# Performance work log

Hardware: AMD Instinct MI355X
Metric: run time of the kernel (lower is better)

## Reference

```python
import jax, jax.numpy as jnp
import numpy as np

L, B, D_MODEL, N_STATE = 512, 32, 256, 16
DT_RANK = 16          # ceil(d_model / 16)
D_INNER = D_MODEL     # EXPAND = 1 (required for code self-consistency)


def setup_inputs() -> dict:
    key = jax.random.key(0)
    ks = jax.random.split(key, 6)
    return {
        "position_features": jax.random.normal(ks[0], (L, B, D_MODEL), jnp.float32),
        "flow_features": jax.random.normal(ks[1], (L, B, D_MODEL), jnp.float32),
        "h_state": jnp.zeros((B, D_INNER, N_STATE), jnp.float32),
        "x_proj_w": jax.random.normal(ks[2], (DT_RANK + 2 * N_STATE, D_INNER), jnp.float32) / np.sqrt(D_INNER).astype(np.float32),
        "dt_proj_w": jax.random.normal(ks[3], (D_INNER, DT_RANK), jnp.float32) / np.sqrt(DT_RANK).astype(np.float32),
        "dt_proj_b": jax.random.normal(ks[4], (D_INNER,), jnp.float32) * 0.01,
        "A_log": jnp.log(jnp.broadcast_to(jnp.arange(1, N_STATE + 1, dtype=jnp.float32), (D_INNER, N_STATE))),
        "D_param": jnp.ones((D_INNER,), jnp.float32),
        "out_proj_w": jax.random.normal(ks[5], (D_MODEL, D_INNER), jnp.float32) / np.sqrt(D_INNER).astype(np.float32),
    }


def _forward(position_features, flow_features, h_state,
             x_proj_w, dt_proj_w, dt_proj_b, A_log, D_param, out_proj_w):
    # permute (L, B, d) -> (B, L, d), matching forward()'s permute(1,0,2)
    u = jnp.transpose(position_features, (1, 0, 2))      # (b, l, d_in)
    flow = jnp.transpose(flow_features, (1, 0, 2))       # (b, l, d_in)

    # input-dependent delta, B, C from flow features
    x_dbl = flow @ x_proj_w.T                            # (b, l, dt_rank + 2n)
    delta, Bm, Cm = jnp.split(x_dbl, [DT_RANK, DT_RANK + N_STATE], axis=-1)
    delta = jax.nn.softplus(delta @ dt_proj_w.T + dt_proj_b)   # (b, l, d_in)

    A = -jnp.exp(A_log)                                  # (d_in, n)
    deltaA = jnp.exp(jnp.einsum('bld,dn->bldn', delta, A))         # (b,l,d,n)
    deltaB_u = jnp.einsum('bld,bln,bld->bldn', delta, Bm, u)       # (b,l,d,n)

    # sequential selective scan over l via lax.scan
    dA_t = jnp.swapaxes(deltaA, 0, 1)                    # (l, b, d, n)
    dBu_t = jnp.swapaxes(deltaB_u, 0, 1)                 # (l, b, d, n)
    C_t = jnp.swapaxes(Cm, 0, 1)                         # (l, b, n)

    def step(h, xs):
        dA, dBu, c = xs
        h = dA * h + dBu                                 # (b, d, n)
        y = jnp.einsum('bdn,bn->bd', h, c)               # (b, d)
        return h, y

    h_final, ys = jax.lax.scan(step, h_state, (dA_t, dBu_t, C_t))
    y = jnp.swapaxes(ys, 0, 1)                           # (b, l, d_in)
    y = y + u * D_param                                  # skip connection

    out = y @ out_proj_w.T                               # (b, l, d_model)
    return out.reshape(out.shape[0], -1), h_final        # flatten(1)


def reference(position_features, flow_features, h_state,
              x_proj_w, dt_proj_w, dt_proj_b, A_log, D_param, out_proj_w):
    return _forward(position_features, flow_features, h_state,
                    x_proj_w, dt_proj_w, dt_proj_b, A_log, D_param, out_proj_w)
```

## Files before the change

kernel.cpp:

```cpp
#include <hip/hip_runtime.h>
#include <hip/hip_bf16.h>

#define LL 512
#define BB 32
#define DD 256
#define NS 16
#define RK 16
#define CH 32
#define LC 16

typedef __attribute__((ext_vector_type(8))) short bf16x8;
typedef __attribute__((ext_vector_type(8))) _Float16 f16x8;
typedef __attribute__((ext_vector_type(4))) float f32x4;

#define LD16(dst, src, off) { \
  float4 _v0 = *reinterpret_cast<const float4*>(&(src)[(off)]); \
  float4 _v1 = *reinterpret_cast<const float4*>(&(src)[(off)+4]); \
  float4 _v2 = *reinterpret_cast<const float4*>(&(src)[(off)+8]); \
  float4 _v3 = *reinterpret_cast<const float4*>(&(src)[(off)+12]); \
  dst[0]=_v0.x; dst[1]=_v0.y; dst[2]=_v0.z; dst[3]=_v0.w; \
  dst[4]=_v1.x; dst[5]=_v1.y; dst[6]=_v1.z; dst[7]=_v1.w; \
  dst[8]=_v2.x; dst[9]=_v2.y; dst[10]=_v2.z; dst[11]=_v2.w; \
  dst[12]=_v3.x; dst[13]=_v3.y; dst[14]=_v3.z; dst[15]=_v3.w; }

#define CP16(dst, src) { _Pragma("unroll") for (int _i = 0; _i < 16; ++_i) dst[_i] = src[_i]; }

static __device__ __forceinline__ unsigned short f2bf(float x) {
    __hip_bfloat16 h = __float2bfloat16(x);
    return *reinterpret_cast<unsigned short*>(&h);
}

static __device__ __forceinline__ f16x8 ld_cvt_f16(const float* p) {
    float4 lo = *reinterpret_cast<const float4*>(p);
    float4 hi = *reinterpret_cast<const float4*>(p + 4);
    f16x8 r;
    r[0] = (_Float16)lo.x; r[1] = (_Float16)lo.y; r[2] = (_Float16)lo.z; r[3] = (_Float16)lo.w;
    r[4] = (_Float16)hi.x; r[5] = (_Float16)hi.y; r[6] = (_Float16)hi.z; r[7] = (_Float16)hi.w;
    return r;
}

__global__ __launch_bounds__(256) void k0_wbf(
    const float* __restrict__ W, unsigned short* __restrict__ Wbf)
{
    int i = (blockIdx.x * 256 + threadIdx.x) * 4;
    float4 v = *reinterpret_cast<const float4*>(&W[i]);
    ushort4 o;
    o.x = f2bf(v.x); o.y = f2bf(v.y); o.z = f2bf(v.z); o.w = f2bf(v.w);
    *reinterpret_cast<ushort4*>(&Wbf[i]) = o;
}

__global__ __launch_bounds__(256) void k0_atab(
    const float* __restrict__ A_log, float* __restrict__ atab, float* __restrict__ atabT)
{
    int i = blockIdx.x * 256 + threadIdx.x;
    int d = i >> 4, n = i & 15;
    float v = -__expf(A_log[i]) * 1.44269504f;
    atab[i] = v;
    atabT[n * DD + d] = v;
}

__global__ __launch_bounds__(256) void k1_fused(
    const float* __restrict__ flow,
    const float* __restrict__ xw,
    const float* __restrict__ dtw,
    const float* __restrict__ dtb,
    float* __restrict__ delta,
    float* __restrict__ Bm,
    float* __restrict__ Cm)
{
    __shared__ float sx16[4][16][17];
    int wave = threadIdx.x >> 6;
    int lane = threadIdx.x & 63;
    int rl = lane & 15, kb = lane >> 4;
    int rowbase = blockIdx.x * 64 + wave * 16;
    int arow = rowbase + rl;
    int b = arow >> 9, l = arow & 511;
    const float* abase = &flow[(l * BB + b) * DD];

    f32x4 acc[3] = {};
    #pragma unroll
    for (int ks = 0; ks < 8; ++ks) {
        int k0 = ks * 32 + kb * 8;
        f16x8 af = ld_cvt_f16(abase + k0);
        #pragma unroll
        for (int j = 0; j < 3; ++j) {
            f16x8 bfr = ld_cvt_f16(&xw[(j * 16 + rl) * DD + k0]);
            acc[j] = __builtin_amdgcn_mfma_f32_16x16x32_f16(af, bfr, acc[j], 0, 0, 0);
        }
    }
    #pragma unroll
    for (int reg = 0; reg < 4; ++reg) {
        int row = rowbase + kb * 4 + reg;
        Bm[(size_t)row * NS + rl] = acc[1][reg];
        Cm[(size_t)row * NS + rl] = acc[2][reg];
        sx16[wave][kb * 4 + reg][rl] = acc[0][reg];
    }
    __syncthreads();

    f16x8 a2;
    if (kb < 2) {
        #pragma unroll
        for (int j = 0; j < 8; ++j)
            a2[j] = (_Float16)sx16[wave][rl][kb * 8 + j];
    } else {
        #pragma unroll
        for (int j = 0; j < 8; ++j) a2[j] = (_Float16)0.f;
    }

    #pragma unroll 4
    for (int m = 0; m < 16; ++m) {
        f16x8 b2;
        if (kb < 2) {
            float4 lo = *reinterpret_cast<const float4*>(&dtw[(m * 16 + rl) * RK + kb * 8]);
            float4 hi = *reinterpret_cast<const float4*>(&dtw[(m * 16 + rl) * RK + kb * 8 + 4]);
            b2[0] = (_Float16)lo.x; b2[1] = (_Float16)lo.y; b2[2] = (_Float16)lo.z; b2[3] = (_Float16)lo.w;
            b2[4] = (_Float16)hi.x; b2[5] = (_Float16)hi.y; b2[6] = (_Float16)hi.z; b2[7] = (_Float16)hi.w;
        } else {
            #pragma unroll
            for (int j = 0; j < 8; ++j) b2[j] = (_Float16)0.f;
        }
        f32x4 acc2 = {};
        acc2 = __builtin_amdgcn_mfma_f32_16x16x32_f16(a2, b2, acc2, 0, 0, 0);
        int d = m * 16 + rl;
        float bias = dtb[d];
        #pragma unroll
        for (int reg = 0; reg < 4; ++reg) {
            float s = acc2[reg] + bias;
            float sp = fmaxf(s, 0.f) + log1pf(__expf(-fabsf(s)));
            delta[(size_t)(rowbase + kb * 4 + reg) * DD + d] = sp;
        }
    }
}

__global__ __launch_bounds__(512, 4) void k2A(
    const float* __restrict__ u_pos,
    const float* __restrict__ atab,
    const float* __restrict__ Dp,
    float* __restrict__ delta,
    const float* __restrict__ Bm,
    const float* __restrict__ Cm,
    float* __restrict__ ypart,
    float* __restrict__ hfin,
    float* __restrict__ sfin)
{
    int tid = threadIdx.x;
    int b  = blockIdx.x >> 4;
    int dt = blockIdx.x & 15;
    int dl = tid & 15, c = tid >> 4;
    int d  = dt * 16 + dl;
    int l0 = c * LC;

    float a[NS];
    LD16(a, atab, d * NS);
    float Dd = Dp[d];

    float* dp = delta + ((size_t)b * LL + l0) * DD + d;
    const float* up = u_pos + ((size_t)l0 * BB + b) * DD + d;
    const float* Bp = Bm + ((size_t)b * LL + l0) * NS;
    const float* Cp = Cm + ((size_t)b * LL + l0) * NS;
    float* yp = ypart + ((size_t)b * LL + l0) * DD + d;

    float h[NS];
    #pragma unroll
    for (int n = 0; n < NS; ++n) h[n] = 0.f;
    float s = 0.f;

    float dlt = dp[0], uv = up[0];
    float Bv[NS], Cv[NS];
    LD16(Bv, Bp, 0);
    LD16(Cv, Cp, 0);

    for (int l = 0; l < LC; ++l) {
        int lp = (l + 1 < LC) ? l + 1 : l;
        float dlt_n = dp[lp * DD];
        float uv_n  = up[lp * BB * DD];
        float Bn[NS], Cn[NS];
        LD16(Bn, Bp, lp * NS);
        LD16(Cn, Cp, lp * NS);

        s += dlt;
        float du = dlt * uv;
        float acc = uv * Dd;
        #pragma unroll
        for (int n = 0; n < NS; ++n) {
            float dA = exp2f(dlt * a[n]);
            h[n] = fmaf(dA, h[n], du * Bv[n]);
            acc = fmaf(h[n], Cv[n], acc);
        }
        yp[l * DD] = acc;
        dp[l * DD] = s;

        dlt = dlt_n; uv = uv_n;
        CP16(Bv, Bn); CP16(Cv, Cn);
    }

    sfin[((size_t)b * CH + c) * DD + d] = s;
    #pragma unroll
    for (int n = 0; n < NS; ++n)
        hfin[(((size_t)b * CH + c) * NS + n) * DD + d] = h[n];
}

__global__ __launch_bounds__(256) void k2B(
    const float* __restrict__ h0,
    const float* __restrict__ atabT,
    const float* __restrict__ sfin,
    float* __restrict__ hfin,
    float* __restrict__ h_out)
{
    int d = threadIdx.x;
    int b = blockIdx.x >> 4;
    int n = blockIdx.x & 15;
    float an = atabT[n * DD + d];
    float s = h0[((size_t)b * DD + d) * NS + n];
    #pragma unroll 4
    for (int c = 0; c < CH; ++c) {
        float sf = sfin[((size_t)b * CH + c) * DD + d];
        size_t oh = (((size_t)b * CH + c) * NS + n) * DD + d;
        float hp = hfin[oh];
        hfin[oh] = s;
        s = fmaf(exp2f(an * sf), s, hp);
    }
    h_out[((size_t)b * DD + d) * NS + n] = s;
}

__global__ __launch_bounds__(256) void k2C(
    const float* __restrict__ atabT,
    const float* __restrict__ Slocal,
    const float* __restrict__ Cm,
    const float* __restrict__ hfin,
    const float* __restrict__ ypart,
    unsigned short* __restrict__ ybf)
{
    int d = threadIdx.x;
    int b = blockIdx.x >> 5;
    int c = blockIdx.x & 31;
    int l0 = c * LC;

    float a[NS], hin[NS];
    #pragma unroll
    for (int n = 0; n < NS; ++n) {
        a[n]   = atabT[n * DD + d];
        hin[n] = hfin[(((size_t)b * CH + c) * NS + n) * DD + d];
    }

    size_t base = ((size_t)b * LL + l0) * DD + d;
    const float* CpB = Cm + ((size_t)b * LL + l0) * NS;

    #pragma unroll 2
    for (int l = 0; l < LC; ++l) {
        float Cv[NS];
        LD16(Cv, CpB, l * NS);
        size_t idx = base + (size_t)l * DD;
        float sS = Slocal[idx];
        float acc = ypart[idx];
        #pragma unroll
        for (int n = 0; n < NS; ++n)
            acc = fmaf(exp2f(a[n] * sS), Cv[n] * hin[n], acc);
        ybf[idx] = f2bf(acc);
    }
}

__global__ __launch_bounds__(256) void k3_mfma(
    const unsigned short* __restrict__ Ybf,
    const unsigned short* __restrict__ Wbf,
    float* __restrict__ Out)
{
    int wave = threadIdx.x >> 6;
    int lane = threadIdx.x & 63;
    int row0 = (blockIdx.x >> 1) * 32 + (wave >> 1) * 16;
    int col0 = (blockIdx.x & 1) * 128 + (wave & 1) * 64;
    int rl = lane & 15, kb = lane >> 4;

    f32x4 acc[4] = {};
    bf16x8 af, bf[4], afn, bfn[4];

    af = *reinterpret_cast<const bf16x8*>(&Ybf[(size_t)(row0 + rl) * DD + kb * 8]);
    #pragma unroll
    for (int j = 0; j < 4; ++j)
        bf[j] = *reinterpret_cast<const bf16x8*>(&Wbf[(size_t)(col0 + j * 16 + rl) * DD + kb * 8]);

    #pragma unroll
    for (int ks = 0; ks < 8; ++ks) {
        int kn = (ks + 1) * 32 + kb * 8;
        if (ks < 7) {
            afn = *reinterpret_cast<const bf16x8*>(&Ybf[(size_t)(row0 + rl) * DD + kn]);
            #pragma unroll
            for (int j = 0; j < 4; ++j)
                bfn[j] = *reinterpret_cast<const bf16x8*>(&Wbf[(size_t)(col0 + j * 16 + rl) * DD + kn]);
        }
        #pragma unroll
        for (int j = 0; j < 4; ++j)
            acc[j] = __builtin_amdgcn_mfma_f32_16x16x32_bf16(af, bf[j], acc[j], 0, 0, 0);
        af = afn;
        #pragma unroll
        for (int j = 0; j < 4; ++j) bf[j] = bfn[j];
    }

    #pragma unroll
    for (int j = 0; j < 4; ++j)
        #pragma unroll
        for (int reg = 0; reg < 4; ++reg)
            Out[(size_t)(row0 + kb * 4 + reg) * DD + col0 + j * 16 + rl] = acc[j][reg];
}

extern "C" void kernel_launch(void* const* d_in, const int* in_sizes, int n_in,
                              void* d_out, int out_size, void* d_ws, size_t ws_size,
                              hipStream_t stream) {
    const float* pos  = (const float*)d_in[0];
    const float* flow = (const float*)d_in[1];
    const float* h0   = (const float*)d_in[2];
    const float* xw   = (const float*)d_in[3];
    const float* dtw  = (const float*)d_in[4];
    const float* dtb  = (const float*)d_in[5];
    const float* alog = (const float*)d_in[6];
    const float* dpar = (const float*)d_in[7];
    const float* ow   = (const float*)d_in[8];

    float* out = (float*)d_out;

    float* ws    = (float*)d_ws;
    float* delta = ws;
    float* Bmw   = ws + 4194304;
    float* Cmw   = ws + 4456448;
    float* ypart = ws + 4718592;
    float* hfin  = ws + 8912896;
    float* sfin  = ws + 13107200;
    float* atab  = ws + 13369344;
    float* atabT = ws + 13373440;
    unsigned short* ybf = (unsigned short*)(ws + 13377536);
    unsigned short* wbf = (unsigned short*)(ws + 15474688);

    float* h_out = out + 32 * 512 * 256;

    k0_wbf  <<<64,   256, 0, stream>>>(ow, wbf);
    k0_atab <<<16,   256, 0, stream>>>(alog, atab, atabT);
    k1_fused<<<256,  256, 0, stream>>>(flow, xw, dtw, dtb, delta, Bmw, Cmw);
    k2A     <<<512,  512, 0, stream>>>(pos, atab, dpar, delta, Bmw, Cmw, ypart, hfin, sfin);
    k2B     <<<512,  256, 0, stream>>>(h0, atabT, sfin, hfin, h_out);
    k2C     <<<1024, 256, 0, stream>>>(atabT, delta, Cmw, hfin, ypart, ybf);
    k3_mfma <<<1024, 256, 0, stream>>>(ybf, wbf, out);
}
```

Before: 214.9 us.

## Fuse chunk correction with output GEMM and split scan state across lanes

New measurement: 214.3 us. About the same (-0.3%).

```diff
diff --git a/kernel.cpp b/kernel.cpp
--- a/kernel.cpp
+++ b/kernel.cpp
@@ -8,8 +8,8 @@
 #define RK 16
 #define CH 32
 #define LC 16
-
-typedef __attribute__((ext_vector_type(8))) short bf16x8;
+#define L2E 1.44269504f
+
 typedef __attribute__((ext_vector_type(8))) _Float16 f16x8;
 typedef __attribute__((ext_vector_type(4))) float f32x4;
 
@@ -23,12 +23,11 @@
   dst[8]=_v2.x; dst[9]=_v2.y; dst[10]=_v2.z; dst[11]=_v2.w; \
   dst[12]=_v3.x; dst[13]=_v3.y; dst[14]=_v3.z; dst[15]=_v3.w; }
 
-#define CP16(dst, src) { _Pragma("unroll") for (int _i = 0; _i < 16; ++_i) dst[_i] = src[_i]; }
-
-static __device__ __forceinline__ unsigned short f2bf(float x) {
-    __hip_bfloat16 h = __float2bfloat16(x);
-    return *reinterpret_cast<unsigned short*>(&h);
-}
+#define LD8(dst, src, off) { \
+  float4 _v0 = *reinterpret_cast<const float4*>(&(src)[(off)]); \
+  float4 _v1 = *reinterpret_cast<const float4*>(&(src)[(off)+4]); \
+  dst[0]=_v0.x; dst[1]=_v0.y; dst[2]=_v0.z; dst[3]=_v0.w; \
+  dst[4]=_v1.x; dst[5]=_v1.y; dst[6]=_v1.z; dst[7]=_v1.w; }
 
 static __device__ __forceinline__ f16x8 ld_cvt_f16(const float* p) {
     float4 lo = *reinterpret_cast<const float4*>(p);
@@ -37,26 +36,6 @@
     r[0] = (_Float16)lo.x; r[1] = (_Float16)lo.y; r[2] = (_Float16)lo.z; r[3] = (_Float16)lo.w;
     r[4] = (_Float16)hi.x; r[5] = (_Float16)hi.y; r[6] = (_Float16)hi.z; r[7] = (_Float16)hi.w;
     return r;
-}
-
-__global__ __launch_bounds__(256) void k0_wbf(
-    const float* __restrict__ W, unsigned short* __restrict__ Wbf)
-{
-    int i = (blockIdx.x * 256 + threadIdx.x) * 4;
-    float4 v = *reinterpret_cast<const float4*>(&W[i]);
-    ushort4 o;
-    o.x = f2bf(v.x); o.y = f2bf(v.y); o.z = f2bf(v.z); o.w = f2bf(v.w);
-    *reinterpret_cast<ushort4*>(&Wbf[i]) = o;
-}
-
-__global__ __launch_bounds__(256) void k0_atab(
-    const float* __restrict__ A_log, float* __restrict__ atab, float* __restrict__ atabT)
-{
-    int i = blockIdx.x * 256 + threadIdx.x;
-    int d = i >> 4, n = i & 15;
-    float v = -__expf(A_log[i]) * 1.44269504f;
-    atab[i] = v;
-    atabT[n * DD + d] = v;
 }
 
 __global__ __launch_bounds__(256) void k1_fused(
@@ -134,7 +113,7 @@
 
 __global__ __launch_bounds__(512, 4) void k2A(
     const float* __restrict__ u_pos,
-    const float* __restrict__ atab,
+    const float* __restrict__ A_log,
     const float* __restrict__ Dp,
     float* __restrict__ delta,
     const float* __restrict__ Bm,
@@ -144,65 +123,65 @@
     float* __restrict__ sfin)
 {
     int tid = threadIdx.x;
-    int b  = blockIdx.x >> 4;
-    int dt = blockIdx.x & 15;
-    int dl = tid & 15, c = tid >> 4;
+    int bid = blockIdx.x;
+    int cg = bid & 1;
+    int dt = (bid >> 1) & 15;
+    int b  = bid >> 5;
+    int dl = tid & 15;
+    int nh = (tid >> 4) & 1;
+    int cl = tid >> 5;
+    int c  = cg * 16 + cl;
     int d  = dt * 16 + dl;
     int l0 = c * LC;
 
-    float a[NS];
-    LD16(a, atab, d * NS);
+    float a[8];
+    LD8(a, A_log, d * NS + nh * 8);
+    #pragma unroll
+    for (int n = 0; n < 8; ++n) a[n] = -__expf(a[n]) * L2E;
     float Dd = Dp[d];
 
     float* dp = delta + ((size_t)b * LL + l0) * DD + d;
     const float* up = u_pos + ((size_t)l0 * BB + b) * DD + d;
-    const float* Bp = Bm + ((size_t)b * LL + l0) * NS;
-    const float* Cp = Cm + ((size_t)b * LL + l0) * NS;
+    const float* Bp = Bm + ((size_t)b * LL + l0) * NS + nh * 8;
+    const float* Cp = Cm + ((size_t)b * LL + l0) * NS + nh * 8;
     float* yp = ypart + ((size_t)b * LL + l0) * DD + d;
 
-    float h[NS];
-    #pragma unroll
-    for (int n = 0; n < NS; ++n) h[n] = 0.f;
+    float h[8];
+    #pragma unroll
+    for (int n = 0; n < 8; ++n) h[n] = 0.f;
     float s = 0.f;
 
-    float dlt = dp[0], uv = up[0];
-    float Bv[NS], Cv[NS];
-    LD16(Bv, Bp, 0);
-    LD16(Cv, Cp, 0);
-
     for (int l = 0; l < LC; ++l) {
-        int lp = (l + 1 < LC) ? l + 1 : l;
-        float dlt_n = dp[lp * DD];
-        float uv_n  = up[lp * BB * DD];
-        float Bn[NS], Cn[NS];
-        LD16(Bn, Bp, lp * NS);
-        LD16(Cn, Cp, lp * NS);
-
+        float dlt = dp[l * DD];
+        float uv  = up[l * BB * DD];
+        float Bv[8], Cv[8];
+        LD8(Bv, Bp, l * NS);
+        LD8(Cv, Cp, l * NS);
         s += dlt;
         float du = dlt * uv;
-        float acc = uv * Dd;
-        #pragma unroll
-        for (int n = 0; n < NS; ++n) {
+        float acc = nh ? 0.f : uv * Dd;
+        #pragma unroll
+        for (int n = 0; n < 8; ++n) {
             float dA = exp2f(dlt * a[n]);
             h[n] = fmaf(dA, h[n], du * Bv[n]);
             acc = fmaf(h[n], Cv[n], acc);
         }
-        yp[l * DD] = acc;
-        dp[l * DD] = s;
-
-        dlt = dlt_n; uv = uv_n;
-        CP16(Bv, Bn); CP16(Cv, Cn);
-    }
-
-    sfin[((size_t)b * CH + c) * DD + d] = s;
-    #pragma unroll
-    for (int n = 0; n < NS; ++n)
-        hfin[(((size_t)b * CH + c) * NS + n) * DD + d] = h[n];
+        acc += __shfl_xor(acc, 16);
+        if (!nh) {
+            yp[l * DD] = acc;
+            dp[l * DD] = s;
+        }
+    }
+
+    if (!nh) sfin[((size_t)b * CH + c) * DD + d] = s;
+    #pragma unroll
+    for (int n = 0; n < 8; ++n)
+        hfin[(((size_t)b * CH + c) * NS + nh * 8 + n) * DD + d] = h[n];
 }
 
 __global__ __launch_bounds__(256) void k2B(
     const float* __restrict__ h0,
-    const float* __restrict__ atabT,
+    const float* __restrict__ A_log,
     const float* __restrict__ sfin,
     float* __restrict__ hfin,
     float* __restrict__ h_out)
@@ -210,7 +189,7 @@
     int d = threadIdx.x;
     int b = blockIdx.x >> 4;
     int n = blockIdx.x & 15;
-    float an = atabT[n * DD + d];
+    float an = -__expf(A_log[d * NS + n]) * L2E;
     float s = h0[((size_t)b * DD + d) * NS + n];
     #pragma unroll 4
     for (int c = 0; c < CH; ++c) {
@@ -223,84 +202,70 @@
     h_out[((size_t)b * DD + d) * NS + n] = s;
 }
 
-__global__ __launch_bounds__(256) void k2C(
-    const float* __restrict__ atabT,
+__global__ __launch_bounds__(512) void k23(
+    const float* __restrict__ A_log,
     const float* __restrict__ Slocal,
     const float* __restrict__ Cm,
     const float* __restrict__ hfin,
     const float* __restrict__ ypart,
-    unsigned short* __restrict__ ybf)
-{
-    int d = threadIdx.x;
-    int b = blockIdx.x >> 5;
-    int c = blockIdx.x & 31;
-    int l0 = c * LC;
-
-    float a[NS], hin[NS];
-    #pragma unroll
-    for (int n = 0; n < NS; ++n) {
-        a[n]   = atabT[n * DD + d];
-        hin[n] = hfin[(((size_t)b * CH + c) * NS + n) * DD + d];
-    }
-
-    size_t base = ((size_t)b * LL + l0) * DD + d;
-    const float* CpB = Cm + ((size_t)b * LL + l0) * NS;
-
-    #pragma unroll 2
-    for (int l = 0; l < LC; ++l) {
-        float Cv[NS];
-        LD16(Cv, CpB, l * NS);
-        size_t idx = base + (size_t)l * DD;
-        float sS = Slocal[idx];
-        float acc = ypart[idx];
-        #pragma unroll
-        for (int n = 0; n < NS; ++n)
-            acc = fmaf(exp2f(a[n] * sS), Cv[n] * hin[n], acc);
-        ybf[idx] = f2bf(acc);
-    }
-}
-
-__global__ __launch_bounds__(256) void k3_mfma(
-    const unsigned short* __restrict__ Ybf,
-    const unsigned short* __restrict__ Wbf,
+    const float* __restrict__ W,
     float* __restrict__ Out)
 {
-    int wave = threadIdx.x >> 6;
-    int lane = threadIdx.x & 63;
-    int row0 = (blockIdx.x >> 1) * 32 + (wave >> 1) * 16;
-    int col0 = (blockIdx.x & 1) * 128 + (wave & 1) * 64;
-    int rl = lane & 15, kb = lane >> 4;
-
-    f32x4 acc[4] = {};
-    bf16x8 af, bf[4], afn, bfn[4];
-
-    af = *reinterpret_cast<const bf16x8*>(&Ybf[(size_t)(row0 + rl) * DD + kb * 8]);
-    #pragma unroll
-    for (int j = 0; j < 4; ++j)
-        bf[j] = *reinterpret_cast<const bf16x8*>(&Wbf[(size_t)(col0 + j * 16 + rl) * DD + kb * 8]);
-
-    #pragma unroll
-    for (int ks = 0; ks < 8; ++ks) {
-        int kn = (ks + 1) * 32 + kb * 8;
-        if (ks < 7) {
-            afn = *reinterpret_cast<const bf16x8*>(&Ybf[(size_t)(row0 + rl) * DD + kn]);
+    __shared__ _Float16 sy[32][264];
+    int tid = threadIdx.x;
+    int b  = blockIdx.x >> 4;
+    int rg = blockIdx.x & 15;
+    int l0 = rg * 32;
+
+    {
+        int d = tid & 255, lgrp = tid >> 8;
+        int c = rg * 2 + lgrp;
+        float a[NS], hin[NS];
+        LD16(a, A_log, d * NS);
+        #pragma unroll
+        for (int n = 0; n < NS; ++n) {
+            a[n] = -__expf(a[n]) * L2E;
+            hin[n] = hfin[(((size_t)b * CH + c) * NS + n) * DD + d];
+        }
+        size_t base = ((size_t)b * LL + l0 + lgrp * 16) * DD + d;
+        const float* Cp = Cm + ((size_t)b * LL + l0 + lgrp * 16) * NS;
+        #pragma unroll 2
+        for (int i = 0; i < 16; ++i) {
+            float Cv[NS];
+            LD16(Cv, Cp, i * NS);
+            size_t idx = base + (size_t)i * DD;
+            float sS = Slocal[idx];
+            float acc = ypart[idx];
             #pragma unroll
-            for (int j = 0; j < 4; ++j)
-                bfn[j] = *reinterpret_cast<const bf16x8*>(&Wbf[(size_t)(col0 + j * 16 + rl) * DD + kn]);
-        }
+            for (int n = 0; n < NS; ++n)
+                acc = fmaf(exp2f(a[n] * sS), Cv[n] * hin[n], acc);
+            sy[lgrp * 16 + i][d] = (_Float16)acc;
+        }
+    }
+    __syncthreads();
+
+    {
+        int wave = tid >> 6, lane = tid & 63;
+        int rl = lane & 15, kb = lane >> 4;
+        int rowg = wave & 1, colg = wave >> 1;
+        f32x4 acc[4] = {};
+        #pragma unroll
+        for (int ks = 0; ks < 8; ++ks) {
+            int k0 = ks * 32 + kb * 8;
+            f16x8 af = *reinterpret_cast<const f16x8*>(&sy[rowg * 16 + rl][k0]);
+            #pragma unroll
+            for (int j = 0; j < 4; ++j) {
+                f16x8 bfr = ld_cvt_f16(&W[(colg * 64 + j * 16 + rl) * DD + k0]);
+                acc[j] = __builtin_amdgcn_mfma_f32_16x16x32_f16(af, bfr, acc[j], 0, 0, 0);
+            }
+        }
+        size_t grow = (size_t)b * LL + l0 + rowg * 16 + kb * 4;
         #pragma unroll
         for (int j = 0; j < 4; ++j)
-            acc[j] = __builtin_amdgcn_mfma_f32_16x16x32_bf16(af, bf[j], acc[j], 0, 0, 0);
-        af = afn;
-        #pragma unroll
-        for (int j = 0; j < 4; ++j) bf[j] = bfn[j];
-    }
-
-    #pragma unroll
-    for (int j = 0; j < 4; ++j)
-        #pragma unroll
-        for (int reg = 0; reg < 4; ++reg)
-            Out[(size_t)(row0 + kb * 4 + reg) * DD + col0 + j * 16 + rl] = acc[j][reg];
+            #pragma unroll
+            for (int reg = 0; reg < 4; ++reg)
+                Out[(grow + reg) * DD + colg * 64 + j * 16 + rl] = acc[j][reg];
+    }
 }
 
 extern "C" void kernel_launch(void* const* d_in, const int* in_sizes, int n_in,
@@ -325,18 +290,11 @@
     float* ypart = ws + 4718592;
     float* hfin  = ws + 8912896;
     float* sfin  = ws + 13107200;
-    float* atab  = ws + 13369344;
-    float* atabT = ws + 13373440;
-    unsigned short* ybf = (unsigned short*)(ws + 13377536);
-    unsigned short* wbf = (unsigned short*)(ws + 15474688);
 
     float* h_out = out + 32 * 512 * 256;
 
-    k0_wbf  <<<64,   256, 0, stream>>>(ow, wbf);
-    k0_atab <<<16,   256, 0, stream>>>(alog, atab, atabT);
     k1_fused<<<256,  256, 0, stream>>>(flow, xw, dtw, dtb, delta, Bmw, Cmw);
-    k2A     <<<512,  512, 0, stream>>>(pos, atab, dpar, delta, Bmw, Cmw, ypart, hfin, sfin);
-    k2B     <<<512,  256, 0, stream>>>(h0, atabT, sfin, hfin, h_out);
-    k2C     <<<1024, 256, 0, stream>>>(atabT, delta, Cmw, hfin, ypart, ybf);
-    k3_mfma <<<1024, 256, 0, stream>>>(ybf, wbf, out);
-}
+    k2A     <<<1024, 512, 0, stream>>>(pos, alog, dpar, delta, Bmw, Cmw, ypart, hfin, sfin);
+    k2B     <<<512,  256, 0, stream>>>(h0, alog, sfin, hfin, h_out);
+    k23     <<<512,  512, 0, stream>>>(alog, delta, Cmw, hfin, ypart, ow, out);
+}
```
